# Performance work log

Hardware: AMD Instinct MI355X
Metric: run time of the kernel (lower is better)

Reference implementation:

```python
import jax, jax.numpy as jnp
import numpy as np
from jax import lax

T, H, I, E = 1024, 1024, 512, 16          # tokens, hidden, moe_intermediate, n_routed_experts
TOP_K, N_GROUP, TOPK_GROUP = 4, 4, 2
N_SHARED = 2
I_SHARED = I * N_SHARED                    # shared-expert intermediate size
ROUTED_SCALE = 2.5


def setup_inputs() -> dict:
    key = jax.random.key(0)
    ks = jax.random.split(key, 9)
    s = lambda k, shape, fan: jax.random.normal(k, shape, jnp.float32) * (fan ** -0.5)
    return {
        "hidden_states": jax.random.normal(ks[0], (T, H), jnp.float32),
        "router_w": s(ks[1], (H, E), H),                 # gate: ReplicatedLinear(H, E)
        "e_bias": jax.random.normal(ks[2], (E,), jnp.float32) * 0.01,  # e_score_correction_bias
        "w_gate": s(ks[3], (E, H, I), H),                # routed experts gate_proj
        "w_up": s(ks[4], (E, H, I), H),                  # routed experts up_proj
        "w_down": s(ks[5], (E, I, H), I),                # routed experts down_proj
        "sw_gate": s(ks[6], (H, I_SHARED), H),           # shared experts gate_proj
        "sw_up": s(ks[7], (H, I_SHARED), H),             # shared experts up_proj
        "sw_down": s(ks[8], (I_SHARED, H), I_SHARED),    # shared experts down_proj
    }


def _grouped_topk_sigmoid(logits, e_bias):
    # DeepSeek-V3 'noaux_tc' grouped top-k with sigmoid scoring.
    scores = jax.nn.sigmoid(logits)                      # [T, E]
    sc = scores + e_bias                                 # biased scores for selection only
    g = sc.reshape(-1, N_GROUP, E // N_GROUP)
    group_scores = lax.top_k(g, 2)[0].sum(-1)            # [T, n_group]: sum of top-2 per group
    _, gidx = lax.top_k(group_scores, TOPK_GROUP)        # [T, topk_group]
    gmask = jax.nn.one_hot(gidx, N_GROUP, dtype=sc.dtype).sum(1)  # [T, n_group]
    emask = jnp.repeat(gmask, E // N_GROUP, axis=1)      # [T, E]
    masked = jnp.where(emask > 0, sc, 0.0)               # sigmoid scores are >=0
    _, tidx = lax.top_k(masked, TOP_K)                   # [T, top_k]
    w = jnp.take_along_axis(scores, tidx, axis=1)        # weights use UNbiased scores
    w = w / (w.sum(-1, keepdims=True) + 1e-20)           # norm_topk_prob=True
    # dense combine weights [T, E]
    combine = (jax.nn.one_hot(tidx, E, dtype=w.dtype) * w[..., None]).sum(1)
    return combine


def reference(hidden_states, router_w, e_bias, w_gate, w_up, w_down,
              sw_gate, sw_up, sw_down):
    x = hidden_states                                    # [T, H]
    logits = x @ router_w                                # [T, E]
    combine = _grouped_topk_sigmoid(logits, e_bias)      # [T, E]

    # routed experts: SiLU-gated MLP per expert, dense-over-experts reference
    gp = jnp.einsum('th,ehi->tei', x, w_gate)            # [T, E, I]
    up = jnp.einsum('th,ehi->tei', x, w_up)
    h = jax.nn.silu(gp) * up
    oe = jnp.einsum('tei,eih->teh', h, w_down)           # [T, E, H]
    routed = jnp.einsum('teh,te->th', oe, combine)       # [T, H]

    # shared experts MLP (reduce_results=False path), fp32 path scales routed only
    shared = (jax.nn.silu(x @ sw_gate) * (x @ sw_up)) @ sw_down  # [T, H]
    return routed * ROUTED_SCALE + shared
```

## Files before the change

kernel.cpp:

```cpp
#include <hip/hip_runtime.h>
#include <stdint.h>

#define T_TOK 1024
#define HDIM  1024
#define IDIM  512
#define NEXP  16
#define ISH   1024
#define MAXTILES 96
#define HSLOTS   5120

typedef _Float16 f16;
typedef __attribute__((ext_vector_type(8))) _Float16 f16x8;
typedef __attribute__((ext_vector_type(4))) _Float16 f16x4;
typedef __attribute__((ext_vector_type(4))) float    f32x4;

__device__ __forceinline__ void gld16(const void* g, void* l) {
  __builtin_amdgcn_global_load_lds(
      (__attribute__((address_space(1))) void*)(uintptr_t)g,
      (__attribute__((address_space(3))) void*)(uint32_t)(uintptr_t)l,
      16, 0, 0);
}

__device__ __forceinline__ f16x8 ldsfrag(const f16* buf, int row, int lch) {
  int phys = lch ^ (row & 7);
  return *(const f16x8*)(buf + row * 64 + phys * 8);
}

__global__ __launch_bounds__(256) void prep_kernel(const float* __restrict__ x,
                                                   f16* __restrict__ xh) {
  int i = blockIdx.x * 256 + threadIdx.x;
  float4 v = ((const float4*)x)[i];
  f16x4 h = { (f16)v.x, (f16)v.y, (f16)v.z, (f16)v.w };
  ((f16x4*)xh)[i] = h;
}

__global__ __launch_bounds__(256) void transpose_all(
    const float* __restrict__ wg, const float* __restrict__ wu, const float* __restrict__ wd,
    const float* __restrict__ sg, const float* __restrict__ su, const float* __restrict__ sd,
    f16* __restrict__ wgT, f16* __restrict__ wuT, f16* __restrict__ wdT,
    f16* __restrict__ sgT, f16* __restrict__ suT, f16* __restrict__ sdT) {
  int z = blockIdx.z;
  const float* src; f16* dst; int R, C;
  if (z < 16)       { src = wg + (size_t)z      * HDIM * IDIM; dst = wgT + (size_t)z      * HDIM * IDIM; R = HDIM; C = IDIM; }
  else if (z < 32)  { src = wu + (size_t)(z-16) * HDIM * IDIM; dst = wuT + (size_t)(z-16) * HDIM * IDIM; R = HDIM; C = IDIM; }
  else if (z < 48)  { src = wd + (size_t)(z-32) * IDIM * HDIM; dst = wdT + (size_t)(z-32) * IDIM * HDIM; R = IDIM; C = HDIM; }
  else if (z == 48) { src = sg; dst = sgT; R = HDIM; C = ISH; }
  else if (z == 49) { src = su; dst = suT; R = HDIM; C = ISH; }
  else              { src = sd; dst = sdT; R = ISH;  C = HDIM; }
  int c0 = blockIdx.x * 64, r0 = blockIdx.y * 64;
  if (c0 >= C || r0 >= R) return;
  __shared__ float tile[64][65];
  int t = threadIdx.x, lc = t & 63, lr0 = t >> 6;
#pragma unroll
  for (int i = 0; i < 16; i++) {
    int lr = lr0 + i * 4;
    tile[lr][lc] = src[(size_t)(r0 + lr) * C + (c0 + lc)];
  }
  __syncthreads();
  int oc = t >> 2, or0 = (t & 3) * 16;
  f16x8 v0, v1;
#pragma unroll
  for (int i = 0; i < 8; i++) {
    v0[i] = (f16)tile[or0 + i][oc];
    v1[i] = (f16)tile[or0 + 8 + i][oc];
  }
  f16* dp = dst + (size_t)(c0 + oc) * R + r0 + or0;
  *(f16x8*)dp = v0;
  *(f16x8*)(dp + 8) = v1;
}

__global__ __launch_bounds__(256) void router_kernel(
    const float* __restrict__ x, const float* __restrict__ rw, const float* __restrict__ ebias,
    int* __restrict__ topk_i, float* __restrict__ topk_w) {
  int wave = threadIdx.x >> 6, l = threadIdx.x & 63;
  int t = blockIdx.x * 4 + wave;
  float acc[16];
#pragma unroll
  for (int e = 0; e < 16; e++) acc[e] = 0.f;
  for (int k = l; k < HDIM; k += 64) {
    float xv = x[(size_t)t * HDIM + k];
    const float4* w4 = (const float4*)(rw + (size_t)k * 16);
#pragma unroll
    for (int q = 0; q < 4; q++) {
      float4 w = w4[q];
      acc[q*4+0] += xv * w.x; acc[q*4+1] += xv * w.y;
      acc[q*4+2] += xv * w.z; acc[q*4+3] += xv * w.w;
    }
  }
#pragma unroll
  for (int off = 32; off >= 1; off >>= 1)
#pragma unroll
    for (int e = 0; e < 16; e++) acc[e] += __shfl_xor(acc[e], off, 64);

  if (l == 0) {
    float s[16], sc[16];
#pragma unroll
    for (int e = 0; e < 16; e++) {
      s[e] = 1.f / (1.f + __expf(-acc[e]));
      sc[e] = s[e] + ebias[e];
    }
    float gs[4];
#pragma unroll
    for (int g = 0; g < 4; g++) {
      float a = -1e30f, b = -1e30f;
#pragma unroll
      for (int j = 0; j < 4; j++) {
        float v = sc[g*4 + j];
        if (v > a) { b = a; a = v; } else if (v > b) { b = v; }
      }
      gs[g] = a + b;
    }
    int g1 = 0;
    for (int g = 1; g < 4; g++) if (gs[g] > gs[g1]) g1 = g;
    int g2 = -1;
    for (int g = 0; g < 4; g++) if (g != g1 && (g2 < 0 || gs[g] > gs[g2])) g2 = g;
    float masked[16];
#pragma unroll
    for (int e = 0; e < 16; e++) {
      int g = e >> 2;
      masked[e] = (g == g1 || g == g2) ? sc[e] : 0.0f;
    }
    int idx[4]; float wv[4]; float denom = 1e-20f;
#pragma unroll
    for (int j = 0; j < 4; j++) {
      int best = 0; float bv = masked[0];
      for (int e = 1; e < 16; e++) if (masked[e] > bv) { bv = masked[e]; best = e; }
      idx[j] = best; wv[j] = s[best]; denom += s[best];
      masked[best] = -1e30f;
    }
#pragma unroll
    for (int j = 0; j < 4; j++) {
      topk_i[t * 4 + j] = idx[j];
      topk_w[t * 4 + j] = wv[j] / denom * 2.5f;
    }
  }
}

__global__ __launch_bounds__(1024) void scatter_kernel(
    const int* __restrict__ tki,
    int* __restrict__ tok, int* __restrict__ slotmap,
    int* __restrict__ tile_e, int* __restrict__ tile_srow,
    int* __restrict__ tile_hb, int* __restrict__ ntl) {
  __shared__ int lcnt[NEXP], lpos[NEXP], lbase[NEXP];
  int t = threadIdx.x;
  if (t < NEXP) { lcnt[t] = 0; lpos[t] = 0; }
  __syncthreads();
  int idx[4];
#pragma unroll
  for (int j = 0; j < 4; j++) idx[j] = tki[t*4+j];
#pragma unroll
  for (int j = 0; j < 4; j++) atomicAdd(&lcnt[idx[j]], 1);
  __syncthreads();
  if (t == 0) {
    int total = 0, slots = 0;
    for (int e = 0; e < NEXP; e++) {
      int c = lcnt[e], nt = (c + 63) >> 6;
      lbase[e] = slots;
      for (int j = 0; j < nt; j++) {
        tile_e[total] = e; tile_srow[total] = j * 64; tile_hb[total] = slots + j * 64; total++;
      }
      slots += nt * 64;
    }
    ntl[0] = total;
  }
  __syncthreads();
#pragma unroll
  for (int j = 0; j < 4; j++) {
    int slot = atomicAdd(&lpos[idx[j]], 1);
    tok[idx[j] * T_TOK + slot] = t;
    slotmap[t * 4 + j] = lbase[idx[j]] + slot;
  }
  __syncthreads();
  int e = t >> 6, s = t & 63;
  int c = lcnt[e];
  int top = ((c + 63) >> 6) << 6;
  if (c + s < top) tok[e * T_TOK + c + s] = 0;
}

__device__ __forceinline__ f32x4 mfma16(f16x8 a, f16x8 b, f32x4 c) {
  return __builtin_amdgcn_mfma_f32_16x16x32_f16(a, b, c, 0, 0, 0);
}

__global__ __launch_bounds__(256) void gu_all(
    const f16* __restrict__ xh,
    const f16* __restrict__ sgT, const f16* __restrict__ suT, f16* __restrict__ hsh,
    const f16* __restrict__ wgT, const f16* __restrict__ wuT, f16* __restrict__ hbuf,
    const int* __restrict__ tile_e, const int* __restrict__ tile_srow,
    const int* __restrict__ tile_hb, const int* __restrict__ ntl,
    const int* __restrict__ tok) {
  int b = blockIdx.x;
  const f16 *Bg, *Bu; f16* Hdst;
  int e = 0, srow = 0, mbase, n0, N;
  bool gather = (b >= 256);
  if (!gather) {
    Bg = sgT; Bu = suT; Hdst = hsh; N = ISH;
    n0 = (b & 15) * 64; mbase = (b >> 4) * 64;
  } else {
    int rb = b - 256, by = rb >> 3;
    if (by >= ntl[0]) return;
    e = tile_e[by]; srow = tile_srow[by]; mbase = tile_hb[by];
    size_t bo = (size_t)e * IDIM * HDIM;
    Bg = wgT + bo; Bu = wuT + bo; Hdst = hbuf; N = IDIM;
    n0 = (rb & 7) * 64;
  }
  const int K = HDIM;

  __shared__ f16 As[64 * 64], Bgs[64 * 64], Bus[64 * 64];

  int tid = threadIdx.x, lane = tid & 63, wave = tid >> 6;
  int quad = lane >> 4, l15 = lane & 15;
  int r = lane >> 3, p = lane & 7;

  const f16* gb[6]; f16* lb[6];
#pragma unroll
  for (int jj = 0; jj < 6; jj++) {
    int j = wave * 6 + jj;
    int buf = j >> 3, i = j & 7;
    int row = i * 8 + r;
    int kcol = (p ^ r) << 3;
    if (buf == 0) {
      int grow = gather ? tok[e * T_TOK + srow + row] : (mbase + row);
      gb[jj] = xh + (size_t)grow * K + kcol;       lb[jj] = (f16*)As + (i << 9);
    } else if (buf == 1) {
      gb[jj] = Bg + (size_t)(n0 + row) * K + kcol; lb[jj] = (f16*)Bgs + (i << 9);
    } else {
      gb[jj] = Bu + (size_t)(n0 + row) * K + kcol; lb[jj] = (f16*)Bus + (i << 9);
    }
  }

  int wr = wave >> 1, wc = wave & 1;
  int ar0 = 32 * wr + l15, br0 = 32 * wc + l15;
  f32x4 zero = {0.f, 0.f, 0.f, 0.f};
  f32x4 aG[2][2] = {{zero, zero}, {zero, zero}};
  f32x4 aU[2][2] = {{zero, zero}, {zero, zero}};

  for (int kt = 0; kt < K; kt += 64) {
    __syncthreads();
#pragma unroll
    for (int jj = 0; jj < 6; jj++) gld16(gb[jj] + kt, lb[jj]);
    __syncthreads();
#pragma unroll
    for (int ks = 0; ks < 2; ks++) {
      int lch = (ks << 2) + quad;
      f16x8 a0 = ldsfrag(As,  ar0,      lch);
      f16x8 a1 = ldsfrag(As,  ar0 + 16, lch);
      f16x8 g0 = ldsfrag(Bgs, br0,      lch);
      f16x8 g1 = ldsfrag(Bgs, br0 + 16, lch);
      f16x8 u0 = ldsfrag(Bus, br0,      lch);
      f16x8 u1 = ldsfrag(Bus, br0 + 16, lch);
      aG[0][0] = mfma16(a0, g0, aG[0][0]); aG[0][1] = mfma16(a0, g1, aG[0][1]);
      aG[1][0] = mfma16(a1, g0, aG[1][0]); aG[1][1] = mfma16(a1, g1, aG[1][1]);
      aU[0][0] = mfma16(a0, u0, aU[0][0]); aU[0][1] = mfma16(a0, u1, aU[0][1]);
      aU[1][0] = mfma16(a1, u0, aU[1][0]); aU[1][1] = mfma16(a1, u1, aU[1][1]);
    }
  }
#pragma unroll
  for (int mi = 0; mi < 2; mi++)
#pragma unroll
    for (int ni = 0; ni < 2; ni++)
#pragma unroll
      for (int rg = 0; rg < 4; rg++) {
        int m = 32 * wr + 16 * mi + (quad << 2) + rg;
        int n = n0 + 32 * wc + 16 * ni + l15;
        float g = aG[mi][ni][rg], u = aU[mi][ni][rg];
        float val = (g / (1.f + __expf(-g))) * u;
        Hdst[(size_t)(mbase + m) * N + n] = (f16)val;
      }
}

__global__ __launch_bounds__(256) void down_all(
    const f16* __restrict__ hsh, const f16* __restrict__ sdT,
    const f16* __restrict__ hbuf, const f16* __restrict__ wdT,
    float* __restrict__ out, float* __restrict__ odown,
    const int* __restrict__ tile_e, const int* __restrict__ tile_srow,
    const int* __restrict__ tile_hb, const int* __restrict__ ntl) {
  int b = blockIdx.x;
  bool routed = (b >= 256);
  const f16 *A, *B; int K, abase, n0, e = 0;
  if (!routed) {
    A = hsh; B = sdT; K = ISH;
    abase = (b >> 4) * 64; n0 = (b & 15) * 64;
  } else {
    int rb = b - 256, by = rb >> 4;
    if (by >= ntl[0]) return;
    e = tile_e[by]; abase = tile_hb[by];
    A = hbuf; B = wdT + (size_t)e * HDIM * IDIM; K = IDIM;
    n0 = (rb & 15) * 64;
  }

  __shared__ f16 As[64 * 64], Bs[64 * 64];

  int tid = threadIdx.x, lane = tid & 63, wave = tid >> 6;
  int quad = lane >> 4, l15 = lane & 15;
  int r = lane >> 3, p = lane & 7;

  const f16* gb[4]; f16* lb[4];
#pragma unroll
  for (int jj = 0; jj < 4; jj++) {
    int j = wave * 4 + jj;
    int buf = j >> 3, i = j & 7;
    int row = i * 8 + r;
    int kcol = (p ^ r) << 3;
    if (buf == 0) { gb[jj] = A + (size_t)(abase + row) * K + kcol; lb[jj] = (f16*)As + (i << 9); }
    else          { gb[jj] = B + (size_t)(n0 + row) * K + kcol;    lb[jj] = (f16*)Bs + (i << 9); }
  }

  int wr = wave >> 1, wc = wave & 1;
  int ar0 = 32 * wr + l15, br0 = 32 * wc + l15;
  f32x4 zero = {0.f, 0.f, 0.f, 0.f};
  f32x4 ac[2][2] = {{zero, zero}, {zero, zero}};

  for (int kt = 0; kt < K; kt += 64) {
    __syncthreads();
#pragma unroll
    for (int jj = 0; jj < 4; jj++) gld16(gb[jj] + kt, lb[jj]);
    __syncthreads();
#pragma unroll
    for (int ks = 0; ks < 2; ks++) {
      int lch = (ks << 2) + quad;
      f16x8 a0 = ldsfrag(As, ar0,      lch);
      f16x8 a1 = ldsfrag(As, ar0 + 16, lch);
      f16x8 b0 = ldsfrag(Bs, br0,      lch);
      f16x8 b1 = ldsfrag(Bs, br0 + 16, lch);
      ac[0][0] = mfma16(a0, b0, ac[0][0]); ac[0][1] = mfma16(a0, b1, ac[0][1]);
      ac[1][0] = mfma16(a1, b0, ac[1][0]); ac[1][1] = mfma16(a1, b1, ac[1][1]);
    }
  }
  float* dst = routed ? odown : out;
#pragma unroll
  for (int mi = 0; mi < 2; mi++)
#pragma unroll
    for (int ni = 0; ni < 2; ni++)
#pragma unroll
      for (int rg = 0; rg < 4; rg++) {
        int m = 32 * wr + 16 * mi + (quad << 2) + rg;
        int n = n0 + 32 * wc + 16 * ni + l15;
        dst[(size_t)(abase + m) * HDIM + n] = ac[mi][ni][rg];
      }
}

__global__ __launch_bounds__(256) void combine_kernel(
    const float* __restrict__ odown, const int* __restrict__ slotmap,
    const float* __restrict__ tkw, float* __restrict__ out) {
  int t = blockIdx.x;
  __shared__ int ss[4]; __shared__ float sw[4];
  if (threadIdx.x < 4) {
    ss[threadIdx.x] = slotmap[t * 4 + threadIdx.x];
    sw[threadIdx.x] = tkw[t * 4 + threadIdx.x];
  }
  __syncthreads();
  int h = threadIdx.x * 4;
  float4 acc = *(const float4*)(out + (size_t)t * HDIM + h);
#pragma unroll
  for (int j = 0; j < 4; j++) {
    float4 v = *(const float4*)(odown + (size_t)ss[j] * HDIM + h);
    float wj = sw[j];
    acc.x += wj * v.x; acc.y += wj * v.y; acc.z += wj * v.z; acc.w += wj * v.w;
  }
  *(float4*)(out + (size_t)t * HDIM + h) = acc;
}

extern "C" void kernel_launch(void* const* d_in, const int* in_sizes, int n_in,
                              void* d_out, int out_size, void* d_ws, size_t ws_size,
                              hipStream_t stream) {
  const float* x  = (const float*)d_in[0];
  const float* rw = (const float*)d_in[1];
  const float* eb = (const float*)d_in[2];
  const float* wg = (const float*)d_in[3];
  const float* wu = (const float*)d_in[4];
  const float* wd = (const float*)d_in[5];
  const float* sg = (const float*)d_in[6];
  const float* su = (const float*)d_in[7];
  const float* sd = (const float*)d_in[8];
  float* out = (float*)d_out;
  (void)in_sizes; (void)n_in; (void)out_size; (void)ws_size;

  char* w = (char*)d_ws;
  size_t off = 0;
  auto alloc = [&](size_t b) { void* p = w + off; off = (off + b + 255) & ~(size_t)255; return p; };

  f16* xh   = (f16*)alloc((size_t)T_TOK * HDIM * 2);
  f16* wgT  = (f16*)alloc((size_t)NEXP * IDIM * HDIM * 2);
  f16* wuT  = (f16*)alloc((size_t)NEXP * IDIM * HDIM * 2);
  f16* wdT  = (f16*)alloc((size_t)NEXP * HDIM * IDIM * 2);
  f16* sgT  = (f16*)alloc((size_t)ISH * HDIM * 2);
  f16* suT  = (f16*)alloc((size_t)ISH * HDIM * 2);
  f16* sdT  = (f16*)alloc((size_t)HDIM * ISH * 2);
  f16* hbuf = (f16*)alloc((size_t)HSLOTS * IDIM * 2);
  f16* hsh  = (f16*)alloc((size_t)T_TOK * ISH * 2);
  int* topk_i = (int*)alloc((size_t)T_TOK * 4 * 4);
  float* topk_w = (float*)alloc((size_t)T_TOK * 4 * 4);
  int* tok  = (int*)alloc((size_t)NEXP * T_TOK * 4);
  int* slotmap = (int*)alloc((size_t)T_TOK * 4 * 4);
  int* tile_e    = (int*)alloc(MAXTILES * 4);
  int* tile_srow = (int*)alloc(MAXTILES * 4);
  int* tile_hb   = (int*)alloc(MAXTILES * 4);
  int* ntl       = (int*)alloc(16);
  float* odown = (float*)wgT;

  prep_kernel<<<1024, 256, 0, stream>>>(x, xh);
  transpose_all<<<dim3(16, 16, 51), 256, 0, stream>>>(wg, wu, wd, sg, su, sd,
                                                      wgT, wuT, wdT, sgT, suT, sdT);
  router_kernel<<<T_TOK / 4, 256, 0, stream>>>(x, rw, eb, topk_i, topk_w);
  scatter_kernel<<<1, 1024, 0, stream>>>(topk_i, tok, slotmap,
                                         tile_e, tile_srow, tile_hb, ntl);
  gu_all<<<256 + (MAXTILES - 16) * 8, 256, 0, stream>>>(
      xh, sgT, suT, hsh, wgT, wuT, hbuf, tile_e, tile_srow, tile_hb, ntl, tok);
  down_all<<<256 + (MAXTILES - 16) * 16, 256, 0, stream>>>(
      hsh, sdT, hbuf, wdT, out, odown, tile_e, tile_srow, tile_hb, ntl);
  combine_kernel<<<T_TOK, 256, 0, stream>>>(odown, slotmap, topk_w, out);
}
```

Measured before the change: 237.7 us.

## Fuse fp16 input cast into router, vectorize transpose loads, store routed down outputs in fp16

```diff
diff --git a/kernel.cpp b/kernel.cpp
--- a/kernel.cpp
+++ b/kernel.cpp
@@ -24,14 +24,6 @@
 __device__ __forceinline__ f16x8 ldsfrag(const f16* buf, int row, int lch) {
   int phys = lch ^ (row & 7);
   return *(const f16x8*)(buf + row * 64 + phys * 8);
-}
-
-__global__ __launch_bounds__(256) void prep_kernel(const float* __restrict__ x,
-                                                   f16* __restrict__ xh) {
-  int i = blockIdx.x * 256 + threadIdx.x;
-  float4 v = ((const float4*)x)[i];
-  f16x4 h = { (f16)v.x, (f16)v.y, (f16)v.z, (f16)v.w };
-  ((f16x4*)xh)[i] = h;
 }
 
 __global__ __launch_bounds__(256) void transpose_all(
@@ -50,11 +42,14 @@
   int c0 = blockIdx.x * 64, r0 = blockIdx.y * 64;
   if (c0 >= C || r0 >= R) return;
   __shared__ float tile[64][65];
-  int t = threadIdx.x, lc = t & 63, lr0 = t >> 6;
-#pragma unroll
-  for (int i = 0; i < 16; i++) {
-    int lr = lr0 + i * 4;
-    tile[lr][lc] = src[(size_t)(r0 + lr) * C + (c0 + lc)];
+  int t = threadIdx.x;
+  int lr = t >> 4, c4 = (t & 15) * 4;
+#pragma unroll
+  for (int pass = 0; pass < 4; pass++) {
+    int r = pass * 16 + lr;
+    float4 v = *(const float4*)(src + (size_t)(r0 + r) * C + (c0 + c4));
+    tile[r][c4 + 0] = v.x; tile[r][c4 + 1] = v.y;
+    tile[r][c4 + 2] = v.z; tile[r][c4 + 3] = v.w;
   }
   __syncthreads();
   int oc = t >> 2, or0 = (t & 3) * 16;
@@ -71,20 +66,29 @@
 
 __global__ __launch_bounds__(256) void router_kernel(
     const float* __restrict__ x, const float* __restrict__ rw, const float* __restrict__ ebias,
-    int* __restrict__ topk_i, float* __restrict__ topk_w) {
+    f16* __restrict__ xh, int* __restrict__ topk_i, float* __restrict__ topk_w) {
   int wave = threadIdx.x >> 6, l = threadIdx.x & 63;
   int t = blockIdx.x * 4 + wave;
   float acc[16];
 #pragma unroll
   for (int e = 0; e < 16; e++) acc[e] = 0.f;
-  for (int k = l; k < HDIM; k += 64) {
-    float xv = x[(size_t)t * HDIM + k];
-    const float4* w4 = (const float4*)(rw + (size_t)k * 16);
-#pragma unroll
-    for (int q = 0; q < 4; q++) {
-      float4 w = w4[q];
-      acc[q*4+0] += xv * w.x; acc[q*4+1] += xv * w.y;
-      acc[q*4+2] += xv * w.z; acc[q*4+3] += xv * w.w;
+#pragma unroll
+  for (int i = 0; i < 4; i++) {
+    int k = i * 256 + l * 4;
+    float4 xv = *(const float4*)(x + (size_t)t * HDIM + k);
+    f16x4 h = { (f16)xv.x, (f16)xv.y, (f16)xv.z, (f16)xv.w };
+    *(f16x4*)(xh + (size_t)t * HDIM + k) = h;
+    const float* xp = &xv.x;
+#pragma unroll
+    for (int j = 0; j < 4; j++) {
+      float xj = xp[j];
+      const float4* w4 = (const float4*)(rw + (size_t)(k + j) * 16);
+#pragma unroll
+      for (int q = 0; q < 4; q++) {
+        float4 w = w4[q];
+        acc[q*4+0] += xj * w.x; acc[q*4+1] += xj * w.y;
+        acc[q*4+2] += xj * w.z; acc[q*4+3] += xj * w.w;
+      }
     }
   }
 #pragma unroll
@@ -271,7 +275,7 @@
 __global__ __launch_bounds__(256) void down_all(
     const f16* __restrict__ hsh, const f16* __restrict__ sdT,
     const f16* __restrict__ hbuf, const f16* __restrict__ wdT,
-    float* __restrict__ out, float* __restrict__ odown,
+    float* __restrict__ out, f16* __restrict__ odown,
     const int* __restrict__ tile_e, const int* __restrict__ tile_srow,
     const int* __restrict__ tile_hb, const int* __restrict__ ntl) {
   int b = blockIdx.x;
@@ -326,7 +330,6 @@
       ac[1][0] = mfma16(a1, b0, ac[1][0]); ac[1][1] = mfma16(a1, b1, ac[1][1]);
     }
   }
-  float* dst = routed ? odown : out;
 #pragma unroll
   for (int mi = 0; mi < 2; mi++)
 #pragma unroll
@@ -335,12 +338,13 @@
       for (int rg = 0; rg < 4; rg++) {
         int m = 32 * wr + 16 * mi + (quad << 2) + rg;
         int n = n0 + 32 * wc + 16 * ni + l15;
-        dst[(size_t)(abase + m) * HDIM + n] = ac[mi][ni][rg];
+        if (routed) odown[(size_t)(abase + m) * HDIM + n] = (f16)ac[mi][ni][rg];
+        else        out  [(size_t)(abase + m) * HDIM + n] = ac[mi][ni][rg];
       }
 }
 
 __global__ __launch_bounds__(256) void combine_kernel(
-    const float* __restrict__ odown, const int* __restrict__ slotmap,
+    const f16* __restrict__ odown, const int* __restrict__ slotmap,
     const float* __restrict__ tkw, float* __restrict__ out) {
   int t = blockIdx.x;
   __shared__ int ss[4]; __shared__ float sw[4];
@@ -353,9 +357,10 @@
   float4 acc = *(const float4*)(out + (size_t)t * HDIM + h);
 #pragma unroll
   for (int j = 0; j < 4; j++) {
-    float4 v = *(const float4*)(odown + (size_t)ss[j] * HDIM + h);
+    f16x4 v = *(const f16x4*)(odown + (size_t)ss[j] * HDIM + h);
     float wj = sw[j];
-    acc.x += wj * v.x; acc.y += wj * v.y; acc.z += wj * v.z; acc.w += wj * v.w;
+    acc.x += wj * (float)v[0]; acc.y += wj * (float)v[1];
+    acc.z += wj * (float)v[2]; acc.w += wj * (float)v[3];
   }
   *(float4*)(out + (size_t)t * HDIM + h) = acc;
 }
@@ -396,12 +401,11 @@
   int* tile_srow = (int*)alloc(MAXTILES * 4);
   int* tile_hb   = (int*)alloc(MAXTILES * 4);
   int* ntl       = (int*)alloc(16);
-  float* odown = (float*)wgT;
-
-  prep_kernel<<<1024, 256, 0, stream>>>(x, xh);
+  f16* odown = (f16*)wgT;
+
   transpose_all<<<dim3(16, 16, 51), 256, 0, stream>>>(wg, wu, wd, sg, su, sd,
                                                       wgT, wuT, wdT, sgT, suT, sdT);
-  router_kernel<<<T_TOK / 4, 256, 0, stream>>>(x, rw, eb, topk_i, topk_w);
+  router_kernel<<<T_TOK / 4, 256, 0, stream>>>(x, rw, eb, xh, topk_i, topk_w);
   scatter_kernel<<<1, 1024, 0, stream>>>(topk_i, tok, slotmap,
                                          tile_e, tile_srow, tile_hb, ntl);
   gu_all<<<256 + (MAXTILES - 16) * 8, 256, 0, stream>>>(
```

Measured after the change: 229.1 us. 3.6% less time.
